# Performance work log

Measured on AMD Instinct MI355X. Metric: run time of the kernel, lower is better.

The kernel has to match this reference:

```python
import jax, jax.numpy as jnp
import numpy as np

H = 8
HID = 512
DH = HID // H
EPS = 1e-5


def _ln(x, g, b):
    mu = jnp.mean(x, axis=-1, keepdims=True)
    var = jnp.mean(jnp.square(x - mu), axis=-1, keepdims=True)
    return (x - mu) * jax.lax.rsqrt(var + EPS) * g + b


def setup_inputs() -> dict:
    key = jax.random.key(0)
    ks = jax.random.split(key, 40)
    L, M, P, D = 4096, 1024, 4096, 512

    def xav(k, shp):
        lim = np.sqrt(6.0 / (shp[0] + shp[1]))
        return jax.random.uniform(k, shp, jnp.float32, -lim, lim)

    inp = {
        'lncRNA_embedding': jax.random.normal(ks[0], (L, D), jnp.float32),
        'miRNA_embedding': jax.random.normal(ks[1], (M, D), jnp.float32),
        'protein_embedding': jax.random.normal(ks[2], (P, D), jnp.float32),
        'lncRNA_miRNA_matrix': jax.random.randint(ks[3], (L, M), 0, 2, jnp.int32),
        'protein_miRNA_matrix': jax.random.randint(ks[4], (P, M), 0, 2, jnp.int32),
    }
    names = ['Wl', 'Wm', 'Wp', 'Wql', 'Wkl', 'Wvl', 'Wqp', 'Wkp', 'Wvp']
    for i, n in enumerate(names):
        inp[n] = xav(ks[5 + i], (HID, HID))
        inp['b' + n[1:]] = jnp.zeros((HID,), jnp.float32)
    inp['Wml'] = xav(ks[20], (2 * HID, D // 2))
    inp['bml'] = jnp.zeros((D // 2,), jnp.float32)
    inp['Wmp'] = xav(ks[21], (2 * HID, D // 2))
    inp['bmp'] = jnp.zeros((D // 2,), jnp.float32)
    inp['g1'] = jnp.ones((D // 2,), jnp.float32)
    inp['be1'] = jnp.zeros((D // 2,), jnp.float32)
    inp['g2'] = jnp.ones((D // 2,), jnp.float32)
    inp['be2'] = jnp.zeros((D // 2,), jnp.float32)
    # first three linears take dim-D input (D == HID here)
    return inp


def reference(lncRNA_embedding, miRNA_embedding, protein_embedding,
              lncRNA_miRNA_matrix, protein_miRNA_matrix,
              Wl, bl, Wm, bm, Wp, bp,
              Wql, bql, Wkl, bkl, Wvl, bvl,
              Wqp, bqp, Wkp, bkp, Wvp, bvp,
              Wml, bml, Wmp, bmp, g1, be1, g2, be2):
    L = lncRNA_embedding.shape[0]
    M = miRNA_embedding.shape[0]
    P = protein_embedding.shape[0]

    lt = lncRNA_embedding @ Wl + bl          # [L, HID]
    mt = miRNA_embedding @ Wm + bm           # [M, HID]
    pt = protein_embedding @ Wp + bp         # [P, HID]

    def heads(x, W, b, n):
        return (x @ W + b).reshape(n, H, DH)

    Ql = heads(lt, Wql, bql, L)              # [L, H, DH]
    Kl = heads(mt, Wkl, bkl, M)
    Vl = heads(mt, Wvl, bvl, M)
    Qp = heads(pt, Wqp, bqp, P)
    Kp = heads(mt, Wkp, bkp, M)
    Vp = heads(mt, Wvp, bvp, M)

    scale = 1.0 / np.sqrt(DH)
    sl = jnp.einsum('lhd,mhd->hlm', Ql, Kl) * scale      # [H, L, M]
    sl = jnp.where(lncRNA_miRNA_matrix[None] == 0, -1e9, sl)
    awl = jax.nn.softmax(sl, axis=-1)

    sp = jnp.einsum('phd,mhd->hpm', Qp, Kp) * scale      # [H, P, M]
    sp = jnp.where(protein_miRNA_matrix[None] == 0, -1e9, sp)
    awp = jax.nn.softmax(sp, axis=-1)

    ctx_l = jax.nn.relu(jnp.einsum('hlm,mhd->lhd', awl, Vl).reshape(L, HID))
    ctx_p = jax.nn.relu(jnp.einsum('hpm,mhd->phd', awp, Vp).reshape(P, HID))

    mutual = jnp.einsum('hlm,hpm->lp', awl, awp) / H     # [L, P]

    fin_l = ctx_l + mutual @ ctx_p
    fin_p = ctx_p + mutual.T @ ctx_l

    out_l = _ln(jnp.concatenate([lt, fin_l], axis=-1) @ Wml + bml, g1, be1)
    out_p = _ln(jnp.concatenate([fin_p, pt], axis=-1) @ Wmp + bmp, g2, be2)
    return out_l, out_p
```

## Files before the change

### kernel.cpp

```cpp
#include <hip/hip_runtime.h>
#include <hip/hip_bf16.h>

using bf16 = __hip_bfloat16;
typedef __attribute__((ext_vector_type(8))) short short8;
typedef __attribute__((ext_vector_type(4))) float floatx4;
typedef __attribute__((ext_vector_type(8))) unsigned short ushort8;
typedef __attribute__((ext_vector_type(4))) int i32x4;
typedef __attribute__((ext_vector_type(8))) int i32x8;

__device__ __forceinline__ float b2f(unsigned short u) {
    union { unsigned int i; float f; } x; x.i = ((unsigned int)u) << 16; return x.f;
}

__device__ __forceinline__ void async16(const void* g, void* l) {
    __builtin_amdgcn_global_load_lds((const __attribute__((address_space(1))) void*)g,
                                     (__attribute__((address_space(3))) void*)l,
                                     16, 0, 0);
}

__device__ __forceinline__ unsigned char f2e4m3(float f) {
    unsigned s = (__float_as_uint(f) >> 24) & 0x80u;
    f = fminf(fabsf(f), 448.f);
    if (f < 0.015625f) {
        int d = (int)rintf(f * 512.f);
        return (unsigned char)(s | (unsigned)d);
    }
    int E = (int)((__float_as_uint(f) >> 23) & 255u) - 127;
    float ulp_inv = __uint_as_float((unsigned)(127 + 3 - E) << 23);
    int m = (int)rintf(f * ulp_inv);
    int n = (m == 16) ? ((E + 8) << 3) : (((E + 7) << 3) + (m - 8));
    if (n > 0x7E) n = 0x7E;
    return (unsigned char)(s | (unsigned)n);
}

__device__ __forceinline__ unsigned int pk4_e4m3(float a, float b, float c, float d) {
#if __has_builtin(__builtin_amdgcn_cvt_pk_fp8_f32)
    int p = __builtin_amdgcn_cvt_pk_fp8_f32(a, b, 0, false);
    p = __builtin_amdgcn_cvt_pk_fp8_f32(c, d, p, true);
    return (unsigned int)p;
#else
    return (unsigned)f2e4m3(a) | ((unsigned)f2e4m3(b) << 8) |
           ((unsigned)f2e4m3(c) << 16) | ((unsigned)f2e4m3(d) << 24);
#endif
}

__device__ __forceinline__ bool sniff_wave(const unsigned short* p) {
    const int lane = threadIdx.x & 63;
    int wild = 0;
#pragma unroll
    for (int j = 0; j < 4; ++j) {
        float a = fabsf(b2f(p[lane * 4 + j]));
        wild += !(a <= 1e4f);
    }
#pragma unroll
    for (int o = 1; o < 64; o <<= 1) wild += __shfl_xor(wild, o);
    return wild > 16;
}

struct Cvt { const void* src; bf16* dst; int n; };
struct PrepArgs {
    Cvt cv[18];
    const void* tsrc[11];
    bf16* tdst[11];
    const unsigned short* sn;
};

__global__ __launch_bounds__(256) void prep(PrepArgs a) {
    const bool f32 = sniff_wave(a.sn);
    const int y = blockIdx.y;
    __shared__ bf16 tile[32][33];

    if (y < 18) {
        const Cvt c = a.cv[y];
        const int stride = gridDim.x * 256 * 8;
        for (int i = (blockIdx.x * 256 + threadIdx.x) * 8; i < c.n; i += stride) {
            if (f32) {
                const float* s = (const float*)c.src + i;
#pragma unroll
                for (int j = 0; j < 8; ++j) c.dst[i + j] = __float2bfloat16(s[j]);
            } else {
                *(ushort8*)((unsigned short*)c.dst + i) =
                    *(const ushort8*)((const unsigned short*)c.src + i);
            }
        }
        return;
    }

    const int tx = threadIdx.x & 31;
    const int ty = threadIdx.x >> 5;
    if (y < 27) {
        const void* in = a.tsrc[y - 18];
        bf16* out = a.tdst[y - 18];
        const int bc = (blockIdx.x & 15) * 32;
        const int br = (blockIdx.x >> 4) * 32;
#pragma unroll
        for (int i = 0; i < 32; i += 8) {
            const size_t idx = (size_t)(br + ty + i) * 512 + bc + tx;
            tile[ty + i][tx] = f32 ? __float2bfloat16(((const float*)in)[idx])
                                   : ((const bf16*)in)[idx];
        }
        __syncthreads();
#pragma unroll
        for (int i = 0; i < 32; i += 8)
            out[(size_t)(bc + ty + i) * 512 + br + tx] = tile[tx][ty + i];
    } else {
        const void* in = a.tsrc[y - 27 + 9];
        bf16* out = a.tdst[y - 27 + 9];
        const int bc = (blockIdx.x & 7) * 32;
        const int br = (blockIdx.x >> 3) * 32;
#pragma unroll
        for (int i = 0; i < 32; i += 8) {
            const size_t idx = (size_t)(br + ty + i) * 256 + bc + tx;
            tile[ty + i][tx] = f32 ? __float2bfloat16(((const float*)in)[idx])
                                   : ((const bf16*)in)[idx];
        }
        __syncthreads();
#pragma unroll
        for (int i = 0; i < 32; i += 8)
            out[(size_t)(bc + ty + i) * 1024 + br + tx] = tile[tx][ty + i];
    }
}

struct SegTab { const bf16* W[3]; const bf16* bias[3]; bf16* C[3]; int ldc[3]; int rs[3]; };

__global__ __launch_bounds__(256) void gemm_bt_seg(
    const bf16* __restrict__ A, SegTab T, int K)
{
    constexpr int TM = 2, TN = 2;
    __align__(16) __shared__ bf16 As[64 * 64];
    __align__(16) __shared__ bf16 Bs[64 * 64];

    const int lane = threadIdx.x & 63;
    const int wv   = threadIdx.x >> 6;
    const int gm   = blockIdx.y * 64;
    const int seg  = (gm >= 5120) ? 2 : ((gm >= 4096) ? 1 : 0);
    const bf16* B  = T.W[seg];
    const bf16* bias = T.bias[seg];
    bf16* C        = T.C[seg];
    const int ldc  = T.ldc[seg];
    const int m_base = gm - T.rs[seg];
    const int n_base = blockIdx.x * 64;
    const int wm0 = (wv >> 1) * 32;
    const int wn0 = (wv & 1) * 32;

    floatx4 zero = {0.f, 0.f, 0.f, 0.f};
    floatx4 acc[TM][TN];
#pragma unroll
    for (int mt = 0; mt < TM; ++mt)
#pragma unroll
        for (int nt = 0; nt < TN; ++nt) acc[mt][nt] = zero;

    const int sr  = lane >> 3;
    const int sce = ((lane & 7) ^ sr) * 8;
    const int fr  = lane & 15;
    const int q   = lane >> 4;
    const int sw  = fr & 7;

    for (int k0 = 0; k0 < K; k0 += 64) {
#pragma unroll
        for (int cc = 0; cc < 2; ++cc) {
            const int r0t = (wv + cc * 4) * 8;
            async16(A + (size_t)(gm + r0t + sr) * 512 + k0 + sce, &As[r0t * 64]);
            async16(B + (size_t)(n_base + r0t + sr) * 512 + k0 + sce, &Bs[r0t * 64]);
        }
        __syncthreads();
#pragma unroll
        for (int s = 0; s < 2; ++s) {
            const int off = ((s * 4 + q) ^ sw) * 8;
            short8 af[TM], bfr[TN];
#pragma unroll
            for (int mt = 0; mt < TM; ++mt)
                af[mt] = *(const short8*)&As[(wm0 + mt * 16 + fr) * 64 + off];
#pragma unroll
            for (int nt = 0; nt < TN; ++nt)
                bfr[nt] = *(const short8*)&Bs[(wn0 + nt * 16 + fr) * 64 + off];
#pragma unroll
            for (int mt = 0; mt < TM; ++mt)
#pragma unroll
                for (int nt = 0; nt < TN; ++nt)
                    acc[mt][nt] = __builtin_amdgcn_mfma_f32_16x16x32_bf16(
                        af[mt], bfr[nt], acc[mt][nt], 0, 0, 0);
        }
        __syncthreads();
    }

    const int er = lane >> 4;
    const int ec = lane & 15;
#pragma unroll
    for (int nt = 0; nt < TN; ++nt) {
        const int col = n_base + wn0 + nt * 16 + ec;
        const float bv = __bfloat162float(bias[col]);
#pragma unroll
        for (int mt = 0; mt < TM; ++mt)
#pragma unroll
            for (int r = 0; r < 4; ++r) {
                const int row = m_base + wm0 + mt * 16 + er * 4 + r;
                C[(size_t)row * ldc + col] = __float2bfloat16(acc[mt][nt][r] + bv);
            }
    }
}

struct BtArgs { const bf16* A; const bf16* B; void* C; const bf16* bias;
                int lda, ldb, ldc; };
struct BtSet { BtArgs s[3]; };

template <bool F32OUT, bool REMAP2>
__global__ __launch_bounds__(256) void gemm_btx(BtSet P, int K, float scale)
{
    constexpr int TM = 2, TN = 2;
    __align__(16) __shared__ bf16 As[64 * 64];
    __align__(16) __shared__ bf16 Bs[64 * 64];

    const BtArgs g = P.s[blockIdx.z];
    int bx = blockIdx.x, by = blockIdx.y;
    if (REMAP2 && blockIdx.z == 2) {
        const int flat = by * gridDim.x + bx;
        bx = flat & 31; by = flat >> 5;
    }
    const int lane = threadIdx.x & 63;
    const int wv   = threadIdx.x >> 6;
    const int m_base = by * 64;
    const int n_base = bx * 64;
    const int wm0 = (wv >> 1) * 32;
    const int wn0 = (wv & 1) * 32;

    floatx4 zero = {0.f, 0.f, 0.f, 0.f};
    floatx4 acc[TM][TN];
#pragma unroll
    for (int mt = 0; mt < TM; ++mt)
#pragma unroll
        for (int nt = 0; nt < TN; ++nt) acc[mt][nt] = zero;

    const int sr  = lane >> 3;
    const int sce = ((lane & 7) ^ sr) * 8;
    const int fr  = lane & 15;
    const int q   = lane >> 4;
    const int sw  = fr & 7;

    for (int k0 = 0; k0 < K; k0 += 64) {
#pragma unroll
        for (int cc = 0; cc < 2; ++cc) {
            const int r0t = (wv + cc * 4) * 8;
            async16(g.A + (size_t)(m_base + r0t + sr) * g.lda + k0 + sce, &As[r0t * 64]);
            async16(g.B + (size_t)(n_base + r0t + sr) * g.ldb + k0 + sce, &Bs[r0t * 64]);
        }
        __syncthreads();
#pragma unroll
        for (int s = 0; s < 2; ++s) {
            const int off = ((s * 4 + q) ^ sw) * 8;
            short8 af[TM], bfr[TN];
#pragma unroll
            for (int mt = 0; mt < TM; ++mt)
                af[mt] = *(const short8*)&As[(wm0 + mt * 16 + fr) * 64 + off];
#pragma unroll
            for (int nt = 0; nt < TN; ++nt)
                bfr[nt] = *(const short8*)&Bs[(wn0 + nt * 16 + fr) * 64 + off];
#pragma unroll
            for (int mt = 0; mt < TM; ++mt)
#pragma unroll
                for (int nt = 0; nt < TN; ++nt)
                    acc[mt][nt] = __builtin_amdgcn_mfma_f32_16x16x32_bf16(
                        af[mt], bfr[nt], acc[mt][nt], 0, 0, 0);
        }
        __syncthreads();
    }

    const int er = lane >> 4;
    const int ec = lane & 15;
#pragma unroll
    for (int nt = 0; nt < TN; ++nt) {
        const int col = n_base + wn0 + nt * 16 + ec;
        const float bv = __bfloat162float(g.bias[col]);
#pragma unroll
        for (int mt = 0; mt < TM; ++mt)
#pragma unroll
            for (int r = 0; r < 4; ++r) {
                const int row = m_base + wm0 + mt * 16 + er * 4 + r;
                const float v = acc[mt][nt][r] * scale + bv;
                if constexpr (F32OUT)
                    ((float*)g.C)[(size_t)row * g.ldc + col] = v;
                else
                    ((bf16*)g.C)[(size_t)row * g.ldc + col] = __float2bfloat16(v);
            }
    }
}

struct ScArgs { const bf16* Q; const bf16* K; const int* mask; unsigned char* aw;
                unsigned char* awt; };
struct ScSet { ScArgs s[2]; const bf16* vsrc[2]; unsigned char* vdst[2]; };

__global__ __launch_bounds__(256) void scores_v8(ScSet P, int ldk, float scale)
{
    __shared__ float wred[16][4];
    __shared__ float wsum[16][4];
    __shared__ float tile[32][33];

    const int flat = blockIdx.x;
    if (flat >= 4096) {
        const int f2   = flat - 4096;
        const int side = f2 >> 9;
        const int rem  = f2 & 511;
        const bf16* in = P.vsrc[side];
        unsigned char* out = P.vdst[side];
        const int bc = (rem & 15) * 32;
        const int br = (rem >> 4) * 32;
        const int tx = threadIdx.x & 31;
        const int ty = threadIdx.x >> 5;
#pragma unroll
        for (int i = 0; i < 32; i += 8)
            tile[ty + i][tx] =
                __bfloat162float(in[(size_t)(br + ty + i) * 2048 + bc + tx]) * 4.0f;
        __syncthreads();
        const unsigned int vp = pk4_e4m3(tile[tx][ty], tile[tx][ty + 8],
                                         tile[tx][ty + 16], tile[tx][ty + 24]);
#pragma unroll
        for (int i = 0; i < 4; ++i)
            out[(size_t)(bc + ty + i * 8) * 1024 + br + tx] =
                (unsigned char)(vp >> (8 * i));
        return;
    }

    const int side = flat >> 11;
    const int idx  = flat & 2047;
    const int h    = idx >> 8;
    const int r0   = (idx & 255) * 16;

    const ScArgs g = P.s[side];
    const int t    = threadIdx.x;
    const int lane = t & 63;
    const int w    = t >> 6;
    const int fr   = lane & 15;
    const int fq   = lane >> 4;
    const int cbase = w * 256;

    const short* Qs = (const short*)g.Q + (size_t)(r0 + fr) * 512 + h * 64 + fq * 8;
    short8 a0 = *(const short8*)(Qs);
    short8 a1 = *(const short8*)(Qs + 32);

    floatx4 accs[16];
    const short* Kb = (const short*)g.K + h * 64 + fq * 8;
#pragma unroll
    for (int c = 0; c < 16; ++c) {
        const int krow = cbase + c * 16 + fr;
        short8 b0 = *(const short8*)(Kb + (size_t)krow * ldk);
        short8 b1 = *(const short8*)(Kb + (size_t)krow * ldk + 32);
        floatx4 acc = {0.f, 0.f, 0.f, 0.f};
        acc = __builtin_amdgcn_mfma_f32_16x16x32_bf16(a0, b0, acc, 0, 0, 0);
        acc = __builtin_amdgcn_mfma_f32_16x16x32_bf16(a1, b1, acc, 0, 0, 0);
        accs[c] = acc;
    }

    float mxr[4] = {-3e38f, -3e38f, -3e38f, -3e38f};
#pragma unroll
    for (int c = 0; c < 16; ++c) {
        const int col = cbase + c * 16 + fr;
#pragma unroll
        for (int r = 0; r < 4; ++r) {
            const int row = r0 + fq * 4 + r;
            float v = (g.mask[(size_t)row * 1024 + col] == 0) ? -1e9f
                                                              : accs[c][r] * scale;
            accs[c][r] = v;
            mxr[r] = fmaxf(mxr[r], v);
        }
    }
#pragma unroll
    for (int o = 1; o < 16; o <<= 1)
#pragma unroll
        for (int r = 0; r < 4; ++r) mxr[r] = fmaxf(mxr[r], __shfl_xor(mxr[r], o));
    if (fr == 0)
#pragma unroll
        for (int r = 0; r < 4; ++r) wred[fq * 4 + r][w] = mxr[r];
    __syncthreads();

    float mx[4], sm[4] = {0.f, 0.f, 0.f, 0.f};
#pragma unroll
    for (int r = 0; r < 4; ++r) {
        const int row = fq * 4 + r;
        mx[r] = fmaxf(fmaxf(wred[row][0], wred[row][1]),
                      fmaxf(wred[row][2], wred[row][3]));
    }
#pragma unroll
    for (int c = 0; c < 16; ++c)
#pragma unroll
        for (int r = 0; r < 4; ++r) {
            float e = __expf(accs[c][r] - mx[r]);
            accs[c][r] = e;
            sm[r] += e;
        }
#pragma unroll
    for (int o = 1; o < 16; o <<= 1)
#pragma unroll
        for (int r = 0; r < 4; ++r) sm[r] += __shfl_xor(sm[r], o);
    if (fr == 0)
#pragma unroll
        for (int r = 0; r < 4; ++r) wsum[fq * 4 + r][w] = sm[r];
    __syncthreads();

    float inv[4];
#pragma unroll
    for (int r = 0; r < 4; ++r) {
        const int row = fq * 4 + r;
        inv[r] = 32.0f / (wsum[row][0] + wsum[row][1] + wsum[row][2] + wsum[row][3]);
    }
    unsigned char* awtb = g.awt + (size_t)(r0 >> 4) * 131072 + fq * 4;
#pragma unroll
    for (int c = 0; c < 16; ++c) {
        const int col = cbase + c * 16 + fr;
        const unsigned int pk = pk4_e4m3(accs[c][0] * inv[0], accs[c][1] * inv[1],
                                         accs[c][2] * inv[2], accs[c][3] * inv[3]);
#pragma unroll
        for (int r = 0; r < 4; ++r)
            g.aw[(size_t)(r0 + fq * 4 + r) * 8192 + h * 1024 + col] =
                (unsigned char)(pk >> (8 * r));
        *(unsigned int*)(awtb + (size_t)(h * 1024 + col) * 16) = pk;
    }
}

struct B8Args { const unsigned char* A; const unsigned char* B; bf16* C;
                unsigned char* CT; };
struct B8Pair { B8Args s[2]; };

__global__ __launch_bounds__(256) void gemm_bt8_ctx(
    B8Pair P, int lda, long long a_kshift, int ldb, int ldc, int ldct,
    int K, float scale)
{
    constexpr int TM = 2, TN = 2;
    __align__(16) __shared__ unsigned char As[64 * 64];
    __align__(16) __shared__ unsigned char Bs[64 * 64];

    const B8Args g = P.s[blockIdx.z];
    const int lane = threadIdx.x & 63;
    const int wv   = threadIdx.x >> 6;
    const int m_base = blockIdx.y * 64;
    const int n_base = blockIdx.x * 64;
    const unsigned char* A = g.A + (long long)blockIdx.x * a_kshift;

    const int wm0 = (wv >> 1) * 32;
    const int wn0 = (wv & 1) * 32;

    floatx4 zero = {0.f, 0.f, 0.f, 0.f};
    floatx4 acc[TM][TN];
#pragma unroll
    for (int mt = 0; mt < TM; ++mt)
#pragma unroll
        for (int nt = 0; nt < TN; ++nt) acc[mt][nt] = zero;

    const int ar = lane >> 2;
    const int ac = (((lane & 3) ^ (ar & 3)) * 16);
    const int fr = lane & 15;
    const int q  = lane >> 4;
    const int sw = fr & 3;

    for (int k0 = 0; k0 < K; k0 += 64) {
        async16(A + (size_t)(m_base + wv * 16 + ar) * lda + k0 + ac, &As[wv * 16 * 64]);
        async16(g.B + (size_t)(n_base + wv * 16 + ar) * ldb + k0 + ac, &Bs[wv * 16 * 64]);
        __syncthreads();
#pragma unroll
        for (int s = 0; s < 2; ++s) {
            const int boff = (((s * 2 + (q >> 1)) ^ sw) * 16) + (q & 1) * 8;
            long af[TM], bfr[TN];
#pragma unroll
            for (int mt = 0; mt < TM; ++mt)
                af[mt] = *(const long*)&As[(wm0 + mt * 16 + fr) * 64 + boff];
#pragma unroll
            for (int nt = 0; nt < TN; ++nt)
                bfr[nt] = *(const long*)&Bs[(wn0 + nt * 16 + fr) * 64 + boff];
#pragma unroll
            for (int mt = 0; mt < TM; ++mt)
#pragma unroll
                for (int nt = 0; nt < TN; ++nt)
                    acc[mt][nt] = __builtin_amdgcn_mfma_f32_16x16x32_fp8_fp8(
                        af[mt], bfr[nt], acc[mt][nt], 0, 0, 0);
        }
        __syncthreads();
    }

    const int er = lane >> 4;
    const int ec = lane & 15;
#pragma unroll
    for (int nt = 0; nt < TN; ++nt) {
        const int col = n_base + wn0 + nt * 16 + ec;
#pragma unroll
        for (int mt = 0; mt < TM; ++mt) {
            const int rowb = m_base + wm0 + mt * 16 + er * 4;
            float v0 = fmaxf(acc[mt][nt][0] * scale, 0.f);
            float v1 = fmaxf(acc[mt][nt][1] * scale, 0.f);
            float v2 = fmaxf(acc[mt][nt][2] * scale, 0.f);
            float v3 = fmaxf(acc[mt][nt][3] * scale, 0.f);
            g.C[(size_t)(rowb + 0) * ldc + col] = __float2bfloat16(v0);
            g.C[(size_t)(rowb + 1) * ldc + col] = __float2bfloat16(v1);
            g.C[(size_t)(rowb + 2) * ldc + col] = __float2bfloat16(v2);
            g.C[(size_t)(rowb + 3) * ldc + col] = __float2bfloat16(v3);
            const unsigned int pk = pk4_e4m3(v0 * 16.f, v1 * 16.f, v2 * 16.f, v3 * 16.f);
            *(unsigned int*)(g.CT + (size_t)col * ldct + rowb) = pk;
        }
    }
}

struct MxArgs { const unsigned char* A; const unsigned char* B; void* C;
                const bf16* Cz; unsigned char* CT; };
struct MxPair { MxArgs s[2]; };

template <int BM, int BN, bool ADDC0, bool FP8OUT, bool TOUT>
__global__ __launch_bounds__(256, 2) void gemm_bt8mx(
    MxPair P, int lda, int ldb, int ldbk, int ldc, int ldc0, int ldct,
    int K, float scale)
{
    constexpr int WM = BM / 2;
    constexpr int WN = BN / 2;
    constexpr int TM = WM / 16;
    constexpr int TN = WN / 16;

    __align__(16) __shared__ unsigned char As[BM * 128];
    __align__(16) __shared__ unsigned char Bs[BN * 128];

    const MxArgs g = P.s[blockIdx.z];
    const int lane = threadIdx.x & 63;
    const int wv   = threadIdx.x >> 6;
    const int m_base = blockIdx.y * BM;
    const int n_base = blockIdx.x * BN;

    const int wm0 = (wv >> 1) * WM;
    const int wn0 = (wv & 1) * WN;

    floatx4 zero = {0.f, 0.f, 0.f, 0.f};
    floatx4 acc[TM][TN];
#pragma unroll
    for (int mt = 0; mt < TM; ++mt)
#pragma unroll
        for (int nt = 0; nt < TN; ++nt) acc[mt][nt] = zero;

    const int sr = lane >> 3;
    const int sc = ((lane & 7) ^ sr) * 16;
    const int fr = lane & 15;
    const int q  = lane >> 4;
    const int sw = fr & 7;

    for (int k0 = 0; k0 < K; k0 += 128) {
#pragma unroll
        for (int cc = 0; cc < BM / 32; ++cc) {
            const int r0t = (wv + cc * 4) * 8;
            async16(g.A + (size_t)(m_base + r0t + sr) * lda + k0 + sc, &As[r0t * 128]);
        }
#pragma unroll
        for (int cc = 0; cc < BN / 32; ++cc) {
            const int r0t = (wv + cc * 4) * 8;
            async16(g.B + (size_t)(n_base + r0t + sr) * ldb +
                        (size_t)((k0 + sc) >> 4) * ldbk, &Bs[r0t * 128]);
        }
        __syncthreads();

        i32x8 af[TM];
#pragma unroll
        for (int mt = 0; mt < TM; ++mt) {
            const unsigned char* rp = &As[(wm0 + mt * 16 + fr) * 128];
            i32x4 lo = *(const i32x4*)(rp + (((q * 2 + 0) ^ sw) * 16));
            i32x4 hi = *(const i32x4*)(rp + (((q * 2 + 1) ^ sw) * 16));
            af[mt] = __builtin_shufflevector(lo, hi, 0, 1, 2, 3, 4, 5, 6, 7);
        }
#pragma unroll
        for (int nt = 0; nt < TN; ++nt) {
            const unsigned char* rp = &Bs[(wn0 + nt * 16 + fr) * 128];
            i32x4 lo = *(const i32x4*)(rp + (((q * 2 + 0) ^ sw) * 16));
            i32x4 hi = *(const i32x4*)(rp + (((q * 2 + 1) ^ sw) * 16));
            i32x8 bf8 = __builtin_shufflevector(lo, hi, 0, 1, 2, 3, 4, 5, 6, 7);
#pragma unroll
            for (int mt = 0; mt < TM; ++mt)
                acc[mt][nt] = __builtin_amdgcn_mfma_scale_f32_16x16x128_f8f6f4(
                    af[mt], bf8, acc[mt][nt], 0, 0, 0, 127, 0, 127);
        }
        __syncthreads();
    }

    const int er = lane >> 4;
    const int ec = lane & 15;
#pragma unroll
    for (int nt = 0; nt < TN; ++nt) {
        const int col = n_base + wn0 + nt * 16 + ec;
#pragma unroll
        for (int mt = 0; mt < TM; ++mt) {
            const int rowb = m_base + wm0 + mt * 16 + er * 4;
            float v[4];
#pragma unroll
            for (int r = 0; r < 4; ++r) {
                v[r] = acc[mt][nt][r] * scale;
                if constexpr (ADDC0)
                    v[r] += __bfloat162float(g.Cz[(size_t)(rowb + r) * ldc0 + col]);
            }
            if constexpr (FP8OUT) {
                const unsigned int pk = pk4_e4m3(v[0], v[1], v[2], v[3]);
#pragma unroll
                for (int r = 0; r < 4; ++r)
                    ((unsigned char*)g.C)[(size_t)(rowb + r) * ldc + col] =
                        (unsigned char)(pk >> (8 * r));
                if constexpr (TOUT)
                    *(unsigned int*)(g.CT + (size_t)col * ldct + rowb) = pk;
            } else {
#pragma unroll
                for (int r = 0; r < 4; ++r)
                    ((bf16*)g.C)[(size_t)(rowb + r) * ldc + col] = __float2bfloat16(v[r]);
            }
        }
    }
}

__global__ __launch_bounds__(256) void ln_all(
    const float* __restrict__ X,
    const bf16* __restrict__ g1, const bf16* __restrict__ be1,
    const bf16* __restrict__ g2, const bf16* __restrict__ be2,
    void* __restrict__ out, const unsigned short* __restrict__ sn)
{
    const bool f32 = sniff_wave(sn);
    const int lane = threadIdx.x & 63;
    const int wv   = threadIdx.x >> 6;
    const int row  = blockIdx.x * 4 + wv;
    const bf16* gg = (row >= 4096) ? g2 : g1;
    const bf16* bb = (row >= 4096) ? be2 : be1;
    const float* x = X + (size_t)row * 256;
    float v[4], s = 0.f, s2 = 0.f;
#pragma unroll
    for (int i = 0; i < 4; ++i) {
        v[i] = x[lane + 64 * i];
        s += v[i]; s2 += v[i] * v[i];
    }
#pragma unroll
    for (int o = 1; o < 64; o <<= 1) { s += __shfl_xor(s, o); s2 += __shfl_xor(s2, o); }
    const float mu  = s * (1.0f / 256.0f);
    const float var = fmaxf(s2 * (1.0f / 256.0f) - mu * mu, 0.0f);
    const float inv = rsqrtf(var + 1e-5f);
#pragma unroll
    for (int i = 0; i < 4; ++i) {
        const int c = lane + 64 * i;
        const float y = (v[i] - mu) * inv * __bfloat162float(gg[c]) + __bfloat162float(bb[c]);
        if (f32) ((float*)out)[(size_t)row * 256 + c] = y;
        else     ((bf16*)out)[(size_t)row * 256 + c] = __float2bfloat16(y);
    }
}

extern "C" void kernel_launch(void* const* d_in, const int* in_sizes, int n_in,
                              void* d_out, int out_size, void* d_ws, size_t ws_size,
                              hipStream_t stream)
{
    const int L = 4096, Mm = 1024, P = 4096;

    const int* mask_l = (const int*)d_in[3];
    const int* mask_p = (const int*)d_in[4];
    const unsigned short* sn = (const unsigned short*)d_in[0];

    char* ws = (char*)d_ws;
    size_t off = 0;
    auto alloc = [&](size_t bytes) {
        void* p = ws + off; off += (bytes + 255) & ~(size_t)255; return p;
    };

    bf16* wt_all = (bf16*)alloc((size_t)9 * 512 * 512 * 2);
    bf16* WmlT   = (bf16*)alloc(1024 * 256 * 2);
    bf16* WmpT   = (bf16*)alloc(1024 * 256 * 2);
    bf16* b_l    = (bf16*)alloc(512 * 2);
    bf16* b_m    = (bf16*)alloc(512 * 2);
    bf16* b_p    = (bf16*)alloc(512 * 2);
    bf16* b_ql   = (bf16*)alloc(512 * 2);
    bf16* b_qp   = (bf16*)alloc(512 * 2);
    bf16* bcat   = (bf16*)alloc(2048 * 2);
    bf16* bml_c  = (bf16*)alloc(256 * 2);
    bf16* bmp_c  = (bf16*)alloc(256 * 2);
    bf16* g1c    = (bf16*)alloc(256 * 2);
    bf16* be1c   = (bf16*)alloc(256 * 2);
    bf16* g2c    = (bf16*)alloc(256 * 2);
    bf16* be2c   = (bf16*)alloc(256 * 2);
    bf16* emb_all = (bf16*)alloc((size_t)(L + Mm + P) * 512 * 2);
    bf16* embl   = emb_all;
    bf16* embm   = emb_all + (size_t)L * 512;
    bf16* embp   = embm + (size_t)Mm * 512;
    bf16* cat_l  = (bf16*)alloc((size_t)L * 1024 * 2);
    bf16* cat_p  = (bf16*)alloc((size_t)P * 1024 * 2);
    bf16* mt     = (bf16*)alloc((size_t)Mm * 512 * 2);
    bf16* Ql     = (bf16*)alloc((size_t)L * 512 * 2);
    bf16* Qp     = (bf16*)alloc((size_t)P * 512 * 2);
    bf16* kvcat  = (bf16*)alloc((size_t)Mm * 2048 * 2);
    unsigned char* V8lT = (unsigned char*)alloc((size_t)512 * Mm);
    unsigned char* V8pT = (unsigned char*)alloc((size_t)512 * Mm);
    bf16* ctx_l  = (bf16*)alloc((size_t)L * 512 * 2);
    bf16* ctx_p  = (bf16*)alloc((size_t)P * 512 * 2);
    unsigned char* ctx8lT = (unsigned char*)alloc((size_t)512 * L);
    unsigned char* ctx8pT = (unsigned char*)alloc((size_t)512 * P);
    unsigned char* awlT8  = (unsigned char*)alloc((size_t)8192 * 4096);
    unsigned char* awpT8  = (unsigned char*)alloc((size_t)8192 * 4096);
    unsigned char* awl8 = (unsigned char*)alloc((size_t)L * 8192);
    unsigned char* awp8 = (unsigned char*)alloc((size_t)P * 8192);
    unsigned char* T1lT = (unsigned char*)emb_all;
    unsigned char* T1pT = (unsigned char*)emb_all + (size_t)512 * 8192;
    float* tmp1 = (float*)awp8;

    PrepArgs pa;
    pa.sn = sn;
    pa.cv[0]  = { d_in[0],  embl, L * 512 };
    pa.cv[1]  = { d_in[1],  embm, Mm * 512 };
    pa.cv[2]  = { d_in[2],  embp, P * 512 };
    pa.cv[3]  = { d_in[6],  b_l,  512 };
    pa.cv[4]  = { d_in[8],  b_m,  512 };
    pa.cv[5]  = { d_in[10], b_p,  512 };
    pa.cv[6]  = { d_in[12], b_ql, 512 };
    pa.cv[7]  = { d_in[18], b_qp, 512 };
    pa.cv[8]  = { d_in[14], bcat,        512 };
    pa.cv[9]  = { d_in[16], bcat + 512,  512 };
    pa.cv[10] = { d_in[20], bcat + 1024, 512 };
    pa.cv[11] = { d_in[22], bcat + 1536, 512 };
    pa.cv[12] = { d_in[24], bml_c, 256 };
    pa.cv[13] = { d_in[26], bmp_c, 256 };
    pa.cv[14] = { d_in[27], g1c,  256 };
    pa.cv[15] = { d_in[28], be1c, 256 };
    pa.cv[16] = { d_in[29], g2c,  256 };
    pa.cv[17] = { d_in[30], be2c, 256 };
    const int slot_of[9] = {0, 1, 2, 3, 5, 6, 4, 7, 8};
    for (int i = 0; i < 9; ++i) {
        pa.tsrc[i] = d_in[5 + 2 * i];
        pa.tdst[i] = wt_all + (size_t)slot_of[i] * 512 * 512;
    }
    pa.tsrc[9]  = d_in[23]; pa.tdst[9]  = WmlT;
    pa.tsrc[10] = d_in[25]; pa.tdst[10] = WmpT;
    prep<<<dim3(256, 29), 256, 0, stream>>>(pa);

    bf16* WlT  = wt_all;
    bf16* WmT  = wt_all + (size_t)1 * 512 * 512;
    bf16* WpT  = wt_all + (size_t)2 * 512 * 512;
    bf16* WqlT = wt_all + (size_t)3 * 512 * 512;
    bf16* WqpT = wt_all + (size_t)4 * 512 * 512;
    bf16* WkvT = wt_all + (size_t)5 * 512 * 512;

    SegTab st;
    st.W[0] = WlT;  st.bias[0] = b_l; st.C[0] = cat_l;       st.ldc[0] = 1024; st.rs[0] = 0;
    st.W[1] = WmT;  st.bias[1] = b_m; st.C[1] = mt;          st.ldc[1] = 512;  st.rs[1] = 4096;
    st.W[2] = WpT;  st.bias[2] = b_p; st.C[2] = cat_p + 512; st.ldc[2] = 1024; st.rs[2] = 5120;
    gemm_bt_seg<<<dim3(8, 144), 256, 0, stream>>>(emb_all, st, 512);

    BtSet qs;
    qs.s[0] = { cat_l,       WqlT, Ql,    b_ql, 1024, 512, 512 };
    qs.s[1] = { cat_p + 512, WqpT, Qp,    b_qp, 1024, 512, 512 };
    qs.s[2] = { mt,          WkvT, kvcat, bcat, 512,  512, 2048 };
    gemm_btx<false, true><<<dim3(8, 64, 3), 256, 0, stream>>>(qs, 512, 1.0f);

    ScSet sc;
    sc.s[0] = { Ql, kvcat,        mask_l, awl8, awlT8 };
    sc.s[1] = { Qp, kvcat + 1024, mask_p, awp8, awpT8 };
    sc.vsrc[0] = kvcat + 512;  sc.vdst[0] = V8lT;
    sc.vsrc[1] = kvcat + 1536; sc.vdst[1] = V8pT;
    scores_v8<<<dim3(5120), 256, 0, stream>>>(sc, 2048, 0.125f);

    B8Pair cx = { { { awl8, V8lT, ctx_l, ctx8lT },
                    { awp8, V8pT, ctx_p, ctx8pT } } };
    gemm_bt8_ctx<<<dim3(8, 64, 2), 256, 0, stream>>>(
        cx, 8192, 1024, 1024, 512, 4096, 1024, 1.0f / 128.0f);

    MxPair t1 = { { { ctx8pT, awpT8, T1lT, nullptr, nullptr },
                    { ctx8lT, awlT8, T1pT, nullptr, nullptr } } };
    gemm_bt8mx<128, 256, false, true, false><<<dim3(32, 4, 2), 256, 0, stream>>>(
        t1, 4096, 16, 131072, 8192, 0, 0, 4096, 1.0f / 128.0f);

    MxPair fn = { { { awl8, T1lT, cat_l + 512, ctx_l, nullptr },
                    { awp8, T1pT, cat_p,       ctx_p, nullptr } } };
    gemm_bt8mx<128, 128, true, false, false><<<dim3(4, 32, 2), 256, 0, stream>>>(
        fn, 8192, 8192, 16, 1024, 512, 0, 8192, 1.0f / 1024.0f);

    BtSet fp;
    fp.s[0] = { cat_l, WmlT, tmp1,                   bml_c, 1024, 1024, 256 };
    fp.s[1] = { cat_p, WmpT, tmp1 + (size_t)L * 256, bmp_c, 1024, 1024, 256 };
    fp.s[2] = fp.s[0];
    gemm_btx<true, false><<<dim3(4, 64, 2), 256, 0, stream>>>(fp, 1024, 1.0f);

    ln_all<<<dim3(2048), 256, 0, stream>>>(tmp1, g1c, be1c, g2c, be2c, d_out, sn);
}
```

Baseline: 477.8 us.

## Pre-pack int32 masks to bytes in prep and interleave heads in scores grid

Adds two extra prep grid rows that convert the int32 lncRNA/protein mask matrices into byte masks, and makes the scores kernel read these byte masks instead of the int32 matrices. The head index now varies fastest in the block index, so the eight head blocks for the same rows run close together and can share the mask in cache. Together these cut mask traffic in scores, which otherwise rereads the 4-byte mask once per head. The cost is a separate pass over the full int32 masks in prep and two extra buffers.

Measured after the change: 481.8 us. About the same (+0.8%).

```diff
diff --git a/kernel.cpp b/kernel.cpp
--- a/kernel.cpp
+++ b/kernel.cpp
@@ -62,14 +62,34 @@
     Cvt cv[18];
     const void* tsrc[11];
     bf16* tdst[11];
+    const int* msrc[2];
+    unsigned char* mdst[2];
     const unsigned short* sn;
 };
 
 __global__ __launch_bounds__(256) void prep(PrepArgs a) {
-    const bool f32 = sniff_wave(a.sn);
     const int y = blockIdx.y;
     __shared__ bf16 tile[32][33];
 
+    if (y >= 29) {
+        const int* src = a.msrc[y - 29];
+        unsigned char* dst = a.mdst[y - 29];
+        const int n = 4096 * 1024;
+        const int stride = gridDim.x * 256 * 16;
+        for (int i = (blockIdx.x * 256 + threadIdx.x) * 16; i < n; i += stride) {
+            union { unsigned char b[16]; i32x4 v; } u;
+#pragma unroll
+            for (int j = 0; j < 4; ++j) {
+                i32x4 m = *(const i32x4*)(src + i + j * 4);
+#pragma unroll
+                for (int k = 0; k < 4; ++k) u.b[j * 4 + k] = m[k] ? 1 : 0;
+            }
+            *(i32x4*)(dst + i) = u.v;
+        }
+        return;
+    }
+
+    const bool f32 = sniff_wave(a.sn);
     if (y < 18) {
         const Cvt c = a.cv[y];
         const int stride = gridDim.x * 256 * 8;
@@ -285,8 +305,8 @@
     }
 }
 
-struct ScArgs { const bf16* Q; const bf16* K; const int* mask; unsigned char* aw;
-                unsigned char* awt; };
+struct ScArgs { const bf16* Q; const bf16* K; const unsigned char* mask;
+                unsigned char* aw; unsigned char* awt; };
 struct ScSet { ScArgs s[2]; const bf16* vsrc[2]; unsigned char* vdst[2]; };
 
 __global__ __launch_bounds__(256) void scores_v8(ScSet P, int ldk, float scale)
@@ -322,8 +342,8 @@
 
     const int side = flat >> 11;
     const int idx  = flat & 2047;
-    const int h    = idx >> 8;
-    const int r0   = (idx & 255) * 16;
+    const int h    = idx & 7;
+    const int r0   = (idx >> 3) * 16;
 
     const ScArgs g = P.s[side];
     const int t    = threadIdx.x;
@@ -688,6 +708,8 @@
     unsigned char* awpT8  = (unsigned char*)alloc((size_t)8192 * 4096);
     unsigned char* awl8 = (unsigned char*)alloc((size_t)L * 8192);
     unsigned char* awp8 = (unsigned char*)alloc((size_t)P * 8192);
+    unsigned char* m8l  = (unsigned char*)alloc((size_t)L * 1024);
+    unsigned char* m8p  = (unsigned char*)alloc((size_t)P * 1024);
     unsigned char* T1lT = (unsigned char*)emb_all;
     unsigned char* T1pT = (unsigned char*)emb_all + (size_t)512 * 8192;
     float* tmp1 = (float*)awp8;
@@ -719,7 +741,9 @@
     }
     pa.tsrc[9]  = d_in[23]; pa.tdst[9]  = WmlT;
     pa.tsrc[10] = d_in[25]; pa.tdst[10] = WmpT;
-    prep<<<dim3(256, 29), 256, 0, stream>>>(pa);
+    pa.msrc[0] = mask_l; pa.mdst[0] = m8l;
+    pa.msrc[1] = mask_p; pa.mdst[1] = m8p;
+    prep<<<dim3(256, 31), 256, 0, stream>>>(pa);
 
     bf16* WlT  = wt_all;
     bf16* WmT  = wt_all + (size_t)1 * 512 * 512;
@@ -741,8 +765,8 @@
     gemm_btx<false, true><<<dim3(8, 64, 3), 256, 0, stream>>>(qs, 512, 1.0f);
 
     ScSet sc;
-    sc.s[0] = { Ql, kvcat,        mask_l, awl8, awlT8 };
-    sc.s[1] = { Qp, kvcat + 1024, mask_p, awp8, awpT8 };
+    sc.s[0] = { Ql, kvcat,        m8l, awl8, awlT8 };
+    sc.s[1] = { Qp, kvcat + 1024, m8p, awp8, awpT8 };
     sc.vsrc[0] = kvcat + 512;  sc.vdst[0] = V8lT;
     sc.vsrc[1] = kvcat + 1536; sc.vdst[1] = V8pT;
     scores_v8<<<dim3(5120), 256, 0, stream>>>(sc, 2048, 0.125f);
```
